# Kernel optimization log

Hardware: AMD Instinct MI355X
Metric: run time of the kernel (lower is better)

The kernel has to match this reference:

```python
import jax, jax.numpy as jnp
import numpy as np

D = 1024
NUM_HEADS = 16
HEAD_SIZE = D // NUM_HEADS  # scaling factor only; no actual head split in original

def setup_inputs() -> dict:
    key = jax.random.key(0)
    ks = jax.random.split(key, 9)
    B, S = 4, 2048
    inp = {
        'incorporacao': jax.random.normal(ks[0], (B, S, D), dtype=jnp.float32),
        'Wq': jax.random.normal(ks[1], (D, D), dtype=jnp.float32) * (1.0 / np.sqrt(D)),
        'bq': jnp.zeros((D,), dtype=jnp.float32),
        'Wk': jax.random.normal(ks[2], (D, D), dtype=jnp.float32) * (1.0 / np.sqrt(D)),
        'bk': jnp.zeros((D,), dtype=jnp.float32),
        'Wv': jax.random.normal(ks[3], (D, D), dtype=jnp.float32) * (1.0 / np.sqrt(D)),
        'bv': jnp.zeros((D,), dtype=jnp.float32),
        'Wo': jax.random.normal(ks[4], (D, D), dtype=jnp.float32) * (1.0 / np.sqrt(D)),
        'bo': jnp.zeros((D,), dtype=jnp.float32),
    }
    return inp

def reference(incorporacao, Wq, bq, Wk, bk, Wv, bv, Wo, bo):
    # Faithful to original: NO head split; attention over full embedding dim,
    # scaled by sqrt(head_size) = sqrt(D / num_cabecas).
    q = jnp.einsum('bsd,df->bsf', incorporacao, Wq) + bq  # [B,S,D]
    k = jnp.einsum('bsd,df->bsf', incorporacao, Wk) + bk
    v = jnp.einsum('bsd,df->bsf', incorporacao, Wv) + bv
    scores = jnp.einsum('bsd,btd->bst', q, k) / jnp.sqrt(jnp.float32(HEAD_SIZE))  # [B,S,S]
    attn = jax.nn.softmax(scores, axis=-1)
    ctx = jnp.einsum('bst,btd->bsd', attn, v)  # [B,S,D]
    out = jnp.einsum('bsd,df->bsf', ctx, Wo) + bo
    return out
```

## Files before the change

kernel.cpp:

```cpp
#include <hip/hip_runtime.h>
#include <cstdint>
#include <cstddef>

typedef unsigned short u16;
typedef __attribute__((ext_vector_type(8))) short short8;
typedef __attribute__((ext_vector_type(4))) float f32x4;

#define BB 4
#define SS 2048
#define DD 1024

__device__ __forceinline__ u16 f2bf(float f) {
  union { float f; unsigned u; } x; x.f = f;
  unsigned r = x.u + 0x7FFFu + ((x.u >> 16) & 1u);
  return (u16)(r >> 16);
}

__device__ __forceinline__ void gld_lds16(const void* g, void* l) {
  __builtin_amdgcn_global_load_lds(
      (const __attribute__((address_space(1))) void*)g,
      (__attribute__((address_space(3))) void*)l, 16, 0, 0);
}

__device__ __forceinline__ void store_out(float* p, float v) { *p = v; }
__device__ __forceinline__ void store_out(u16* p, float v) { *p = f2bf(v); }

template<typename OutT, int BN, int MODE, bool HAS_BIAS>
__global__ __launch_bounds__(512, 2) void gemm8p(
    const u16* __restrict__ A, size_t sA, int ldaB,
    const u16* __restrict__ B, size_t sB, int ldbB,
    OutT* __restrict__ C, size_t sC, int ldc,
    const float* __restrict__ bias, float scale, int K,
    u16* __restrict__ out2, u16* __restrict__ out3)
{
  constexpr int NFR   = BN / 64;
  constexpr int BSLOT = BN * 32;
  __shared__ u16 sm[32768 + 4 * BSLOT];

  const int gx = gridDim.x, gy = gridDim.y;
  const int nwg = gx * gy * gridDim.z;
  const int flat = blockIdx.x + gx * (blockIdx.y + gy * blockIdx.z);
  const int swz = (flat & 7) * (nwg >> 3) + (flat >> 3);
  const int bz  = swz / (gx * gy);
  const int rem = swz - bz * (gx * gy);
  const int by  = rem / gx;
  const int bx  = rem - by * gx;
  const int blockM = by * 256, blockN = bx * BN;

  const char* Abase = (const char*)(A + (size_t)bz * sA);
  const char* Bbase = (const char*)(B + (size_t)bz * sB);

  const int tid  = threadIdx.x;
  const int wave = tid >> 6, lane = tid & 63;
  const int wrow = (wave >> 2) * 128;
  const int wcol = (wave & 3) * (BN / 4);

  const int sr  = tid >> 2;
  const int scb = ((tid & 3) * 16) ^ (((sr >> 1) & 3) << 4);
  const char* gA0 = Abase + (size_t)(blockM + sr)       * ldaB + scb;
  const char* gA1 = Abase + (size_t)(blockM + sr + 128) * ldaB + scb;
  const char* gB0 = Bbase + (size_t)(blockN + sr)       * ldbB + scb;
  const char* gB1 = gB0;
  if constexpr (BN == 256) gB1 = Bbase + (size_t)(blockN + sr + 128) * ldbB + scb;
  const int ldsw = wave * 512;

  const int r16 = lane & 15, q8 = (lane >> 4) * 8;
  int offA[8], offB[NFR];
#pragma unroll
  for (int mi = 0; mi < 8; ++mi) {
    const int row = wrow + mi * 16 + r16;
    offA[mi] = row * 32 + (q8 ^ (((row >> 1) & 3) << 3));
  }
#pragma unroll
  for (int nj = 0; nj < NFR; ++nj) {
    const int row = wcol + nj * 16 + r16;
    offB[nj] = row * 32 + (q8 ^ (((row >> 1) & 3) << 3));
  }

  auto STAGE = [&](int r, int kb) {
    gld_lds16(gA0 + kb, sm + r * 8192 + ldsw);
    gld_lds16(gA1 + kb, sm + r * 8192 + 4096 + ldsw);
    gld_lds16(gB0 + kb, sm + 32768 + r * BSLOT + ldsw);
    if constexpr (BN == 256)
      gld_lds16(gB1 + kb, sm + 32768 + r * BSLOT + 4096 + ldsw);
  };

  f32x4 acc[8][NFR] = {};
  const int NT = K >> 6;

  STAGE(0, 0);
  STAGE(1, 64);
  if constexpr (BN == 256) asm volatile("s_waitcnt vmcnt(4)" ::: "memory");
  else                     asm volatile("s_waitcnt vmcnt(3)" ::: "memory");
  __builtin_amdgcn_s_barrier();

  for (int t = 0; t < NT; ++t) {
#pragma unroll
    for (int kh = 0; kh < 2; ++kh) {
      const int ring = (2 * t + kh) & 3;
      const u16* As = sm + ring * 8192;
      const u16* Bs = sm + 32768 + ring * BSLOT;

      short8 af[8], bfv[NFR];
#pragma unroll
      for (int mi = 0; mi < 8; ++mi) af[mi] = *(const short8*)(As + offA[mi]);
#pragma unroll
      for (int nj = 0; nj < NFR; ++nj) bfv[nj] = *(const short8*)(Bs + offB[nj]);

      if (t + 1 < NT) {
        STAGE((ring + 2) & 3, (t + 1) * 128 + kh * 64);
        if constexpr (BN == 256) asm volatile("s_waitcnt vmcnt(4)" ::: "memory");
        else                     asm volatile("s_waitcnt vmcnt(3)" ::: "memory");
      } else {
        asm volatile("s_waitcnt vmcnt(0)" ::: "memory");
      }
      __builtin_amdgcn_s_barrier();
      asm volatile("s_waitcnt lgkmcnt(0)" ::: "memory");
      __builtin_amdgcn_sched_barrier(0);

      __builtin_amdgcn_s_setprio(1);
#pragma unroll
      for (int mi = 0; mi < 8; ++mi)
#pragma unroll
        for (int nj = 0; nj < NFR; ++nj)
          acc[mi][nj] = __builtin_amdgcn_mfma_f32_16x16x32_bf16(
              af[mi], bfv[nj], acc[mi][nj], 0, 0, 0);
      __builtin_amdgcn_s_setprio(0);
      __builtin_amdgcn_s_barrier();
    }
  }

  const int cr = lane & 15, rr0 = (lane >> 4) * 4;
  OutT* Cb = C + (size_t)bz * sC;
#pragma unroll
  for (int nj = 0; nj < NFR; ++nj) {
    const int colg = blockN + wcol + nj * 16 + cr;
    const float bval = HAS_BIAS ? bias[colg] : 0.0f;
#pragma unroll
    for (int mi = 0; mi < 8; ++mi) {
      f32x4 v = acc[mi][nj];
      const int rowg = blockM + wrow + mi * 16 + rr0;
      if constexpr (MODE == 0) {
#pragma unroll
        for (int i = 0; i < 4; ++i)
          store_out(&Cb[(size_t)(rowg + i) * ldc + colg], v[i] * scale + bval);
      } else {
        if (colg < 2048) {
          u16* dst = (colg < 1024) ? (u16*)Cb : out2;
          const int c2 = colg & 1023;
#pragma unroll
          for (int i = 0; i < 4; ++i)
            dst[(size_t)(rowg + i) * 1024 + c2] = f2bf(v[i] + bval);
        } else {
          const int d  = colg - 2048;
          const int b  = rowg >> 11;
          const int t0 = rowg & 2047;
          u16 h0 = f2bf(v[0] + bval), h1 = f2bf(v[1] + bval);
          u16 h2 = f2bf(v[2] + bval), h3 = f2bf(v[3] + bval);
          uint2 u;
          u.x = (unsigned)h0 | ((unsigned)h1 << 16);
          u.y = (unsigned)h2 | ((unsigned)h3 << 16);
          *(uint2*)&out3[((size_t)b * 1024 + d) * 2048 + t0] = u;
        }
      }
    }
  }
}

__global__ __launch_bounds__(256) void cvt_f32_bf16(
    const float* __restrict__ in, u16* __restrict__ out, int n4)
{
  int i = blockIdx.x * 256 + threadIdx.x;
  if (i >= n4) return;
  float4 v = ((const float4*)in)[i];
  uint2 u;
  u.x = (unsigned)f2bf(v.x) | ((unsigned)f2bf(v.y) << 16);
  u.y = (unsigned)f2bf(v.z) | ((unsigned)f2bf(v.w) << 16);
  ((uint2*)out)[i] = u;
}

__global__ __launch_bounds__(256) void transpose_cvt(
    const float* __restrict__ W, u16* __restrict__ Wt)
{
  __shared__ u16 tile[32][33];
  const int tx = threadIdx.x;
  const int ty = threadIdx.y;
  const int bx = blockIdx.x * 32;
  const int by = blockIdx.y * 32;
#pragma unroll
  for (int j = 0; j < 4; ++j) {
    int d = by + ty * 4 + j;
    tile[ty * 4 + j][tx] = f2bf(W[(size_t)d * DD + bx + tx]);
  }
  __syncthreads();
#pragma unroll
  for (int j = 0; j < 4; ++j) {
    int f = bx + ty * 4 + j;
    Wt[(size_t)f * DD + by + tx] = tile[tx][ty * 4 + j];
  }
}

__global__ __launch_bounds__(256) void concat_bias(
    const float* __restrict__ bq, const float* __restrict__ bk,
    const float* __restrict__ bv, float* __restrict__ out)
{
  int i = blockIdx.x * 256 + threadIdx.x;
  const float* src = (i < 1024) ? bq : ((i < 2048) ? bk : bv);
  out[i] = src[i & 1023];
}

__global__ __launch_bounds__(256) void softmax_inplace(float* __restrict__ S)
{
  const int tid = threadIdx.x;
  float* rp = S + (size_t)blockIdx.x * SS;

  float4 v0 = ((const float4*)rp)[tid];
  float4 v1 = ((const float4*)rp)[tid + 256];

  float m = fmaxf(fmaxf(fmaxf(v0.x, v0.y), fmaxf(v0.z, v0.w)),
                  fmaxf(fmaxf(v1.x, v1.y), fmaxf(v1.z, v1.w)));
#pragma unroll
  for (int off = 32; off; off >>= 1) m = fmaxf(m, __shfl_xor(m, off));

  __shared__ float smax[4];
  __shared__ float ssum[4];
  const int wave = tid >> 6, lane = tid & 63;
  if (lane == 0) smax[wave] = m;
  __syncthreads();
  m = fmaxf(fmaxf(smax[0], smax[1]), fmaxf(smax[2], smax[3]));

  float e[8];
  e[0] = __expf(v0.x - m); e[1] = __expf(v0.y - m);
  e[2] = __expf(v0.z - m); e[3] = __expf(v0.w - m);
  e[4] = __expf(v1.x - m); e[5] = __expf(v1.y - m);
  e[6] = __expf(v1.z - m); e[7] = __expf(v1.w - m);
  float s = e[0] + e[1] + e[2] + e[3] + e[4] + e[5] + e[6] + e[7];
#pragma unroll
  for (int off = 32; off; off >>= 1) s += __shfl_xor(s, off);
  if (lane == 0) ssum[wave] = s;
  __syncthreads();
  float inv = 1.0f / (ssum[0] + ssum[1] + ssum[2] + ssum[3]);

  uint2 u0, u1;
  u0.x = (unsigned)f2bf(e[0] * inv) | ((unsigned)f2bf(e[1] * inv) << 16);
  u0.y = (unsigned)f2bf(e[2] * inv) | ((unsigned)f2bf(e[3] * inv) << 16);
  u1.x = (unsigned)f2bf(e[4] * inv) | ((unsigned)f2bf(e[5] * inv) << 16);
  u1.y = (unsigned)f2bf(e[6] * inv) | ((unsigned)f2bf(e[7] * inv) << 16);
  ((uint2*)rp)[tid]       = u0;
  ((uint2*)rp)[tid + 256] = u1;
}

extern "C" void kernel_launch(void* const* d_in, const int* in_sizes, int n_in,
                              void* d_out, int out_size, void* d_ws, size_t ws_size,
                              hipStream_t stream) {
  (void)in_sizes; (void)n_in; (void)out_size; (void)ws_size;
  const float* X  = (const float*)d_in[0];
  const float* Wq = (const float*)d_in[1];
  const float* bq = (const float*)d_in[2];
  const float* Wk = (const float*)d_in[3];
  const float* bk = (const float*)d_in[4];
  const float* Wv = (const float*)d_in[5];
  const float* bv = (const float*)d_in[6];
  const float* Wo = (const float*)d_in[7];
  const float* bo = (const float*)d_in[8];

  char* ws = (char*)d_ws;
  const size_t MBy = 1ull << 20;
  u16*   Xbf   = (u16*)(ws + 0);
  u16*   WtAll = (u16*)(ws + 16 * MBy);
  u16*   Wto   = (u16*)(ws + 22 * MBy);
  u16*   Qb    = (u16*)(ws + 24 * MBy);
  u16*   Kb    = (u16*)(ws + 40 * MBy);
  u16*   Vt    = (u16*)(ws + 56 * MBy);
  float* Sf    = (float*)(ws + 72 * MBy);
  float* bqkv  = (float*)(ws + 72 * MBy);
  u16*   Ctx   = (u16*)(ws + 136 * MBy);

  cvt_f32_bf16<<<dim3((BB * SS * DD / 4) / 256), 256, 0, stream>>>(X, Xbf, BB * SS * DD / 4);
  dim3 tb(32, 8);
  transpose_cvt<<<dim3(32, 32), tb, 0, stream>>>(Wq, WtAll);
  transpose_cvt<<<dim3(32, 32), tb, 0, stream>>>(Wk, WtAll + 1024 * 1024);
  transpose_cvt<<<dim3(32, 32), tb, 0, stream>>>(Wv, WtAll + 2 * 1024 * 1024);
  transpose_cvt<<<dim3(32, 32), tb, 0, stream>>>(Wo, Wto);
  concat_bias<<<dim3(12), 256, 0, stream>>>(bq, bk, bv, bqkv);

  gemm8p<u16, 128, 1, true><<<dim3(24, 32, 1), 512, 0, stream>>>(
      Xbf, 0, DD * 2, WtAll, 0, DD * 2,
      Qb, 0, 0, bqkv, 1.0f, DD, Kb, Vt);

  gemm8p<float, 256, 0, false><<<dim3(8, 8, BB), 512, 0, stream>>>(
      Qb, (size_t)SS * DD, DD * 2, Kb, (size_t)SS * DD, DD * 2,
      Sf, (size_t)SS * SS, SS, nullptr, 0.125f, DD, nullptr, nullptr);

  softmax_inplace<<<dim3(BB * SS), 256, 0, stream>>>(Sf);

  gemm8p<u16, 128, 0, false><<<dim3(8, 8, BB), 512, 0, stream>>>(
      (const u16*)Sf, (size_t)SS * 2 * SS, 2 * SS * 2,
      Vt, (size_t)DD * SS, SS * 2,
      Ctx, (size_t)SS * DD, DD, nullptr, 1.0f, SS, nullptr, nullptr);

  gemm8p<float, 128, 0, true><<<dim3(8, 32, 1), 512, 0, stream>>>(
      Ctx, 0, DD * 2, Wto, 0, DD * 2,
      (float*)d_out, 0, DD, bo, 1.0f, DD, nullptr, nullptr);
}
```

Before: 224.0 us.

## Restructure GEMM to fixed 256-wide N tile with 3-deep single-barrier pipeline

The GEMM template now fixes the N tile at 256 and makes the M tile variable (128 or 256), so grids are re-shaped for the QKV, P·V and output projections. The main loop now steps over 32-wide K slices with three stages in flight. It uses one barrier per slice instead of two and issues the next prefetch after the barrier, overlapping global→LDS loads with MFMA work. This cuts barrier overhead and deepens prefetch, but changes tile shapes and occupancy, and the counted vmcnt waits must match exactly or data races appear.

```diff
diff --git a/kernel.cpp b/kernel.cpp
--- a/kernel.cpp
+++ b/kernel.cpp
@@ -25,7 +25,7 @@
 __device__ __forceinline__ void store_out(float* p, float v) { *p = v; }
 __device__ __forceinline__ void store_out(u16* p, float v) { *p = f2bf(v); }
 
-template<typename OutT, int BN, int MODE, bool HAS_BIAS>
+template<typename OutT, int BM, int MODE, bool HAS_BIAS>
 __global__ __launch_bounds__(512, 2) void gemm8p(
     const u16* __restrict__ A, size_t sA, int ldaB,
     const u16* __restrict__ B, size_t sB, int ldbB,
@@ -33,9 +33,11 @@
     const float* __restrict__ bias, float scale, int K,
     u16* __restrict__ out2, u16* __restrict__ out3)
 {
-  constexpr int NFR   = BN / 64;
-  constexpr int BSLOT = BN * 32;
-  __shared__ u16 sm[32768 + 4 * BSLOT];
+  constexpr int MF    = BM / 32;
+  constexpr int ASLOT = BM * 32;
+  constexpr int ASETS = BM / 128;
+  constexpr int L     = ASETS + 2;
+  __shared__ u16 sm[4 * ASLOT + 4 * 8192];
 
   const int gx = gridDim.x, gy = gridDim.y;
   const int nwg = gx * gy * gridDim.z;
@@ -45,99 +47,92 @@
   const int rem = swz - bz * (gx * gy);
   const int by  = rem / gx;
   const int bx  = rem - by * gx;
-  const int blockM = by * 256, blockN = bx * BN;
+  const int blockM = by * BM, blockN = bx * 256;
 
   const char* Abase = (const char*)(A + (size_t)bz * sA);
   const char* Bbase = (const char*)(B + (size_t)bz * sB);
 
   const int tid  = threadIdx.x;
   const int wave = tid >> 6, lane = tid & 63;
-  const int wrow = (wave >> 2) * 128;
-  const int wcol = (wave & 3) * (BN / 4);
+  const int wrow = (wave >> 2) * (BM / 2);
+  const int wcol = (wave & 3) * 64;
 
   const int sr  = tid >> 2;
   const int scb = ((tid & 3) * 16) ^ (((sr >> 1) & 3) << 4);
-  const char* gA0 = Abase + (size_t)(blockM + sr)       * ldaB + scb;
-  const char* gA1 = Abase + (size_t)(blockM + sr + 128) * ldaB + scb;
+  const char* gA0 = Abase + (size_t)(blockM + sr) * ldaB + scb;
+  const char* gA1 = (ASETS == 2) ? Abase + (size_t)(blockM + sr + 128) * ldaB + scb
+                                 : nullptr;
   const char* gB0 = Bbase + (size_t)(blockN + sr)       * ldbB + scb;
-  const char* gB1 = gB0;
-  if constexpr (BN == 256) gB1 = Bbase + (size_t)(blockN + sr + 128) * ldbB + scb;
+  const char* gB1 = Bbase + (size_t)(blockN + sr + 128) * ldbB + scb;
   const int ldsw = wave * 512;
 
+  auto STAGE = [&](int r) {
+    gld_lds16(gA0, sm + r * ASLOT + ldsw);
+    if constexpr (ASETS == 2) gld_lds16(gA1, sm + r * ASLOT + 4096 + ldsw);
+    gld_lds16(gB0, sm + 4 * ASLOT + r * 8192 + ldsw);
+    gld_lds16(gB1, sm + 4 * ASLOT + r * 8192 + 4096 + ldsw);
+    gA0 += 64; gB0 += 64; gB1 += 64;
+    if constexpr (ASETS == 2) gA1 += 64;
+  };
+
   const int r16 = lane & 15, q8 = (lane >> 4) * 8;
-  int offA[8], offB[NFR];
-#pragma unroll
-  for (int mi = 0; mi < 8; ++mi) {
+  int offA[MF], offB[4];
+#pragma unroll
+  for (int mi = 0; mi < MF; ++mi) {
     const int row = wrow + mi * 16 + r16;
     offA[mi] = row * 32 + (q8 ^ (((row >> 1) & 3) << 3));
   }
 #pragma unroll
-  for (int nj = 0; nj < NFR; ++nj) {
+  for (int nj = 0; nj < 4; ++nj) {
     const int row = wcol + nj * 16 + r16;
     offB[nj] = row * 32 + (q8 ^ (((row >> 1) & 3) << 3));
   }
 
-  auto STAGE = [&](int r, int kb) {
-    gld_lds16(gA0 + kb, sm + r * 8192 + ldsw);
-    gld_lds16(gA1 + kb, sm + r * 8192 + 4096 + ldsw);
-    gld_lds16(gB0 + kb, sm + 32768 + r * BSLOT + ldsw);
-    if constexpr (BN == 256)
-      gld_lds16(gB1 + kb, sm + 32768 + r * BSLOT + 4096 + ldsw);
-  };
-
-  f32x4 acc[8][NFR] = {};
-  const int NT = K >> 6;
-
-  STAGE(0, 0);
-  STAGE(1, 64);
-  if constexpr (BN == 256) asm volatile("s_waitcnt vmcnt(4)" ::: "memory");
-  else                     asm volatile("s_waitcnt vmcnt(3)" ::: "memory");
+  f32x4 acc[MF][4] = {};
+  const int NP = K >> 5;
+
+  STAGE(0); STAGE(1); STAGE(2);
+  asm volatile("s_waitcnt vmcnt(%0)" :: "i"(2 * L) : "memory");
   __builtin_amdgcn_s_barrier();
-
-  for (int t = 0; t < NT; ++t) {
-#pragma unroll
-    for (int kh = 0; kh < 2; ++kh) {
-      const int ring = (2 * t + kh) & 3;
-      const u16* As = sm + ring * 8192;
-      const u16* Bs = sm + 32768 + ring * BSLOT;
-
-      short8 af[8], bfv[NFR];
-#pragma unroll
-      for (int mi = 0; mi < 8; ++mi) af[mi] = *(const short8*)(As + offA[mi]);
-#pragma unroll
-      for (int nj = 0; nj < NFR; ++nj) bfv[nj] = *(const short8*)(Bs + offB[nj]);
-
-      if (t + 1 < NT) {
-        STAGE((ring + 2) & 3, (t + 1) * 128 + kh * 64);
-        if constexpr (BN == 256) asm volatile("s_waitcnt vmcnt(4)" ::: "memory");
-        else                     asm volatile("s_waitcnt vmcnt(3)" ::: "memory");
-      } else {
-        asm volatile("s_waitcnt vmcnt(0)" ::: "memory");
-      }
-      __builtin_amdgcn_s_barrier();
-      asm volatile("s_waitcnt lgkmcnt(0)" ::: "memory");
-      __builtin_amdgcn_sched_barrier(0);
-
-      __builtin_amdgcn_s_setprio(1);
-#pragma unroll
-      for (int mi = 0; mi < 8; ++mi)
-#pragma unroll
-        for (int nj = 0; nj < NFR; ++nj)
-          acc[mi][nj] = __builtin_amdgcn_mfma_f32_16x16x32_bf16(
-              af[mi], bfv[nj], acc[mi][nj], 0, 0, 0);
-      __builtin_amdgcn_s_setprio(0);
-      __builtin_amdgcn_s_barrier();
-    }
+  __builtin_amdgcn_sched_barrier(0);
+
+  for (int p = 0; p < NP; ++p) {
+    const int ring = p & 3;
+    const u16* As = sm + ring * ASLOT;
+    const u16* Bs = sm + 4 * ASLOT + ring * 8192;
+
+    short8 bfv[4], af[MF];
+#pragma unroll
+    for (int nj = 0; nj < 4; ++nj) bfv[nj] = *(const short8*)(Bs + offB[nj]);
+#pragma unroll
+    for (int mi = 0; mi < MF; ++mi) af[mi] = *(const short8*)(As + offA[mi]);
+
+    if (p < NP - 2)       asm volatile("s_waitcnt vmcnt(%0)" :: "i"(L) : "memory");
+    else if (p == NP - 2) asm volatile("s_waitcnt vmcnt(0)" ::: "memory");
+    __builtin_amdgcn_s_barrier();
+    __builtin_amdgcn_sched_barrier(0);
+
+    if (p + 3 < NP) STAGE((p + 3) & 3);
+
+    __builtin_amdgcn_s_setprio(1);
+#pragma unroll
+    for (int mi = 0; mi < MF; ++mi)
+#pragma unroll
+      for (int nj = 0; nj < 4; ++nj)
+        acc[mi][nj] = __builtin_amdgcn_mfma_f32_16x16x32_bf16(
+            af[mi], bfv[nj], acc[mi][nj], 0, 0, 0);
+    __builtin_amdgcn_s_setprio(0);
+    __builtin_amdgcn_sched_barrier(0);
   }
 
   const int cr = lane & 15, rr0 = (lane >> 4) * 4;
   OutT* Cb = C + (size_t)bz * sC;
 #pragma unroll
-  for (int nj = 0; nj < NFR; ++nj) {
+  for (int nj = 0; nj < 4; ++nj) {
     const int colg = blockN + wcol + nj * 16 + cr;
     const float bval = HAS_BIAS ? bias[colg] : 0.0f;
 #pragma unroll
-    for (int mi = 0; mi < 8; ++mi) {
+    for (int mi = 0; mi < MF; ++mi) {
       f32x4 v = acc[mi][nj];
       const int rowg = blockM + wrow + mi * 16 + rr0;
       if constexpr (MODE == 0) {
@@ -284,7 +279,7 @@
   transpose_cvt<<<dim3(32, 32), tb, 0, stream>>>(Wo, Wto);
   concat_bias<<<dim3(12), 256, 0, stream>>>(bq, bk, bv, bqkv);
 
-  gemm8p<u16, 128, 1, true><<<dim3(24, 32, 1), 512, 0, stream>>>(
+  gemm8p<u16, 256, 1, true><<<dim3(12, 32, 1), 512, 0, stream>>>(
       Xbf, 0, DD * 2, WtAll, 0, DD * 2,
       Qb, 0, 0, bqkv, 1.0f, DD, Kb, Vt);
 
@@ -294,12 +289,12 @@
 
   softmax_inplace<<<dim3(BB * SS), 256, 0, stream>>>(Sf);
 
-  gemm8p<u16, 128, 0, false><<<dim3(8, 8, BB), 512, 0, stream>>>(
+  gemm8p<u16, 128, 0, false><<<dim3(4, 16, BB), 512, 0, stream>>>(
       (const u16*)Sf, (size_t)SS * 2 * SS, 2 * SS * 2,
       Vt, (size_t)DD * SS, SS * 2,
       Ctx, (size_t)SS * DD, DD, nullptr, 1.0f, SS, nullptr, nullptr);
 
-  gemm8p<float, 128, 0, true><<<dim3(8, 32, 1), 512, 0, stream>>>(
+  gemm8p<float, 128, 0, true><<<dim3(4, 64, 1), 512, 0, stream>>>(
       Ctx, 0, DD * 2, Wto, 0, DD * 2,
       (float*)d_out, 0, DD, bo, 1.0f, DD, nullptr, nullptr);
 }
```

Result: faster. 216.6 us (-3.3%).
